# Performance work log

Measured on AMD Instinct MI355X. Metric: run time of the kernel, lower is better.

## Reference

```python
import jax, jax.numpy as jnp
import numpy as np
from functools import partial

N = 10  # n_qubits (static)


def _rx(state, w, theta, n):
    # state: [B, 2^n] complex64; RX(theta) on wire w (wire 0 = most significant)
    B = state.shape[0]
    st = state.reshape(B, 2 ** w, 2, 2 ** (n - 1 - w))
    half = jnp.asarray(theta, state.real.dtype) * 0.5
    c = jnp.cos(half).reshape(-1, 1, 1)
    s = jnp.sin(half).reshape(-1, 1, 1)
    s0, s1 = st[:, :, 0], st[:, :, 1]
    n0 = c * s0 - 1j * s * s1
    n1 = -1j * s * s0 + c * s1
    return jnp.stack([n0, n1], axis=2).reshape(B, 2 ** n)


def _cnot(state, control, target, n):
    B = state.shape[0]
    a, bb = (control, target) if control < target else (target, control)
    st = state.reshape(B, 2 ** a, 2, 2 ** (bb - a - 1), 2, 2 ** (n - 1 - bb))
    if control == a:
        # control is axis 2, target axis 4: flip target where control==1
        c1 = jnp.flip(st[:, :, 1], axis=3)
        st = jnp.stack([st[:, :, 0], c1], axis=2)
    else:
        # control is axis 4, target axis 2: flip axis-2 slice where control==1
        c1 = jnp.flip(st[:, :, :, :, 1], axis=1)
        st = jnp.stack([st[:, :, :, :, 0], c1], axis=4)
    return st.reshape(B, 2 ** n)


def _expect_z(state, n):
    B = state.shape[0]
    probs = jnp.abs(state) ** 2  # [B, 2^n]
    es = []
    for w in range(n):
        p = probs.reshape(B, 2 ** w, 2, 2 ** (n - 1 - w))
        es.append(p[:, :, 0].sum((1, 2)) - p[:, :, 1].sum((1, 2)))
    return jnp.stack(es, axis=1)  # [B, n]


def _qlayer(x, theta, n):
    # x: [B, n] encoder angles; theta: [n] trainable RX angles
    B = x.shape[0]
    state = jnp.zeros((B, 2 ** n), jnp.complex64).at[:, 0].set(1.0)
    for w in range(n):
        state = _rx(state, w, x[:, w], n)
    for w in range(n):
        state = _rx(state, w, theta[w], n)
    for w in range(n - 1):
        state = _cnot(state, w, w + 1, n)
    state = _cnot(state, n - 1, 0, n)
    return _expect_z(state, n)


def setup_inputs() -> dict:
    key = jax.random.key(0)
    k1, k2, k3, k4 = jax.random.split(key, 4)
    T, B, D, H = 64, 256, 246, N
    inputs = jax.random.normal(k1, (T, B, D), jnp.float32)
    fan_in = D + H
    W = jax.random.normal(k2, (4, N, fan_in), jnp.float32) / np.sqrt(fan_in)
    b = jax.random.normal(k3, (4, N), jnp.float32) * 0.01
    thetas = jax.random.normal(k4, (4, N), jnp.float32)
    return {"inputs": inputs, "W": W, "b": b, "thetas": thetas}


def reference(inputs, W, b, thetas):
    T, B, D = inputs.shape
    H = thetas.shape[-1]
    qlayer4 = jax.vmap(partial(_qlayer, n=N))  # over the 4 gates

    def step(carry, x_t):
        hx, cx = carry
        comb = jnp.concatenate([x_t, hx], axis=1)          # [B, D+H]
        z = jnp.einsum('bi,goi->gbo', comb, W) + b[:, None, :]  # [4, B, n]
        gates = qlayer4(z, thetas)                          # [4, B, n]
        f = jax.nn.sigmoid(gates[0])
        i = jax.nn.sigmoid(gates[1])
        g = jnp.tanh(gates[2])
        o = jax.nn.sigmoid(gates[3])
        cx = f * cx + i * g
        hx = o * jnp.tanh(cx)
        return (hx, cx), hx

    hx0 = jnp.zeros((B, H), inputs.dtype)
    cx0 = jnp.zeros((B, H), inputs.dtype)
    (hx, cx), outputs = jax.lax.scan(step, (hx0, cx0), inputs)
    return outputs, hx, cx
```

## Files before the change

### kernel.cpp

```cpp
#include <hip/hip_runtime.h>
#include <hip/hip_bf16.h>

#define D_IN   246
#define NW     10
#define NG     4
#define FANIN  256
#define BATCH  256
#define TSTEPS 64
#define ZSTR   42
#define WP_ELEMS (NG * D_IN * 16)

__global__ __launch_bounds__(256) void k_wt(const float* __restrict__ W,
                                            float* __restrict__ Wp) {
    int e = blockIdx.x * 256 + threadIdx.x;
    if (e >= WP_ELEMS) return;
    int o = e & 15;
    int i = (e >> 4) % D_IN;
    int g = e / (16 * D_IN);
    float v = (o < NW) ? W[(g * NW + o) * FANIN + i] : 0.f;
    Wp[e] = v;
}

template <int CTRL>
__device__ __forceinline__ float dpp_shr_mul(float p) {
    int up = __builtin_amdgcn_update_dpp(__float_as_int(1.0f), __float_as_int(p),
                                         CTRL, 0xF, 0xF, false);
    return p * __int_as_float(up);
}

__global__ __launch_bounds__(256) void k_fused(
    const float* __restrict__ x,
    const float* __restrict__ Wp,
    const float* __restrict__ bias,
    const float* __restrict__ theta,
    const float* __restrict__ W,
    float* __restrict__ out,
    float* __restrict__ hxout,
    float* __restrict__ cxout)
{
    const int b    = blockIdx.x;
    const int tid  = threadIdx.x;
    const int lane = tid & 63;
    const int wv   = __builtin_amdgcn_readfirstlane(tid >> 6);

    __shared__ float xl[64 * D_IN];
    __shared__ float zl[TSTEPS * ZSTR];

    for (int row = wv; row < 64; row += 4) {
        const float* src = x + ((size_t)row * BATCH + b) * D_IN;
        float* dst = xl + row * D_IN;
        for (int j = lane; j < 123; j += 64) {
            float2 v = *reinterpret_cast<const float2*>(src + 2 * j);
            *reinterpret_cast<float2*>(dst + 2 * j) = v;
        }
    }
    __syncthreads();

    {
        const int g = wv;
        float acc[NW];
#pragma unroll
        for (int o = 0; o < NW; ++o)
            acc[o] = bias[g * NW + o] + theta[g * NW + o];

        const float* wg = Wp + g * D_IN * 16;
        const float* xr = xl + lane * D_IN;

#pragma unroll 4
        for (int ii = 0; ii < 123; ++ii) {
            float2 xv = *reinterpret_cast<const float2*>(xr + 2 * ii);
#pragma unroll
            for (int o = 0; o < NW; ++o) {
                acc[o] = fmaf(xv.x, wg[(2 * ii) * 16 + o], acc[o]);
                acc[o] = fmaf(xv.y, wg[(2 * ii + 1) * 16 + o], acc[o]);
            }
        }

        float* zo = zl + lane * ZSTR + g * NW;
#pragma unroll
        for (int q = 0; q < 5; ++q)
            *reinterpret_cast<float2*>(zo + 2 * q) = make_float2(acc[2 * q], acc[2 * q + 1]);
    }
    __syncthreads();

    if (wv != 0) return;

    const int r   = lane >> 4;
    const int o   = lane & 15;
    const bool act = (o < NW);
    const int oc  = act ? o : 0;
    const int cidx = r * NW + oc;

    float wh[NW];
#pragma unroll
    for (int j = 0; j < NW; ++j)
        wh[j] = W[(r * NW + oc) * FANIN + D_IN + j];

    const float am = (r == 2) ? 2.f : 1.f;
    const float vm = (r == 2) ? 2.f : 1.f;
    const float vc = (r == 2) ? -1.f : 0.f;
    const int idx1 = (lane ^ 16) << 2;
    const int idx2 = (lane ^ 32) << 2;
    const int idx3 = (lane ^ 48) << 2;
    const bool q1 = (r & 1) != 0;
    const bool q2 = (r & 2) != 0;

    float hx_s[NW];
#pragma unroll
    for (int j = 0; j < NW; ++j) hx_s[j] = 0.f;

    float cx = 0.f, hv = 0.f;
    float zc = zl[cidx];

    for (int t = 0; t < TSTEPS; ++t) {
        float zn = zl[((t + 1) & 63) * ZSTR + cidx];

        float s0 = zc, s1 = 0.f;
#pragma unroll
        for (int j = 0; j < 5; ++j) {
            s0 = fmaf(hx_s[2 * j],     wh[2 * j],     s0);
            s1 = fmaf(hx_s[2 * j + 1], wh[2 * j + 1], s1);
        }
        float z = s0 + s1;

        float cv = __cosf(z);

        float p = cv;
        p = dpp_shr_mul<0x111>(p);
        p = dpp_shr_mul<0x112>(p);
        p = dpp_shr_mul<0x114>(p);
        p = dpp_shr_mul<0x118>(p);

        float e  = __expf(-(p * am));
        float sg = __fdividef(1.f, 1.f + e);
        float val = fmaf(sg, vm, vc);

        int vi = __float_as_int(val);
        float a1 = __int_as_float(__builtin_amdgcn_ds_bpermute(idx1, vi));
        float a2 = __int_as_float(__builtin_amdgcn_ds_bpermute(idx2, vi));
        float a3 = __int_as_float(__builtin_amdgcn_ds_bpermute(idx3, vi));

        float fv = q2 ? (q1 ? a3 : a2) : (q1 ? a1 : val);
        float iv = q2 ? (q1 ? a2 : a3) : (q1 ? val : a1);
        float gv = q2 ? (q1 ? a1 : val) : (q1 ? a3 : a2);
        float ov = q2 ? (q1 ? val : a1) : (q1 ? a2 : a3);

        cx = fmaf(fv, cx, iv * gv);
        float e2 = __expf(cx + cx);
        float th = 1.f - __fdividef(2.f, 1.f + e2);
        hv = ov * th;

        if (r == 0 && act) out[((size_t)t * BATCH + b) * NW + o] = hv;

#pragma unroll
        for (int j = 0; j < NW; ++j)
            hx_s[j] = __int_as_float(__builtin_amdgcn_readlane(__float_as_int(hv), j));

        zc = zn;
    }

    if (r == 0 && act) {
        hxout[b * NW + o] = hv;
        cxout[b * NW + o] = cx;
    }
}

extern "C" void kernel_launch(void* const* d_in, const int* in_sizes, int n_in,
                              void* d_out, int out_size, void* d_ws, size_t ws_size,
                              hipStream_t stream) {
    const float* x     = (const float*)d_in[0];
    const float* W     = (const float*)d_in[1];
    const float* bias  = (const float*)d_in[2];
    const float* theta = (const float*)d_in[3];

    float* out   = (float*)d_out;
    float* hxout = out + (size_t)TSTEPS * BATCH * NW;
    float* cxout = hxout + (size_t)BATCH * NW;

    float* Wp = (float*)d_ws;

    k_wt<<<(WP_ELEMS + 255) / 256, 256, 0, stream>>>(W, Wp);
    k_fused<<<BATCH, 256, 0, stream>>>(x, Wp, bias, theta, W, out, hxout, cxout);
}
```

Before: 121.8 us.

## Split input projection across 8 waves and compute all four gates per lane

The kernel now launches 512 threads per block, splitting the 246-wide input projection into two K-halves across 8 waves and reducing the partial sums through shared memory. The recurrent phase is restructured so each lane evaluates all four gates for its hidden unit. This replaces the cross-row ds_bpermute exchange with four independent cos/DPP product chains, and the four z values are read as one float4 from a gate-interleaved LDS layout. The goal is to shorten the precompute phase and the serial per-step latency. The cost is an extra barrier, more LDS use, and more per-lane work in the recurrence.

```diff
diff --git a/kernel.cpp b/kernel.cpp
--- a/kernel.cpp
+++ b/kernel.cpp
@@ -4,10 +4,10 @@
 #define D_IN   246
 #define NW     10
 #define NG     4
+#define NOUT   40
 #define FANIN  256
 #define BATCH  256
 #define TSTEPS 64
-#define ZSTR   42
 #define WP_ELEMS (NG * D_IN * 16)
 
 __global__ __launch_bounds__(256) void k_wt(const float* __restrict__ W,
@@ -28,7 +28,7 @@
     return p * __int_as_float(up);
 }
 
-__global__ __launch_bounds__(256) void k_fused(
+__global__ __launch_bounds__(512) void k_fused(
     const float* __restrict__ x,
     const float* __restrict__ Wp,
     const float* __restrict__ bias,
@@ -42,11 +42,25 @@
     const int tid  = threadIdx.x;
     const int lane = tid & 63;
     const int wv   = __builtin_amdgcn_readfirstlane(tid >> 6);
+    const int g    = wv & 3;
+    const int kh   = wv >> 2;
 
     __shared__ float xl[64 * D_IN];
-    __shared__ float zl[TSTEPS * ZSTR];
+    __shared__ float pr[NG][64][NW];
+    __shared__ float zl[TSTEPS * NOUT];
 
-    for (int row = wv; row < 64; row += 4) {
+    const int o16 = lane & 15;
+    const int oc  = (o16 < NW) ? o16 : 0;
+    float wh[NG][NW];
+    if (wv == 0) {
+#pragma unroll
+        for (int gg = 0; gg < NG; ++gg)
+#pragma unroll
+            for (int j = 0; j < NW; ++j)
+                wh[gg][j] = W[(gg * NW + oc) * FANIN + D_IN + j];
+    }
+
+    for (int row = wv; row < 64; row += 8) {
         const float* src = x + ((size_t)row * BATCH + b) * D_IN;
         float* dst = xl + row * D_IN;
         for (int j = lane; j < 123; j += 64) {
@@ -57,111 +71,96 @@
     __syncthreads();
 
     {
-        const int g = wv;
+        const int khbase = kh ? 124 : 0;
+        const int npairs = kh ? 61 : 62;
+
         float acc[NW];
 #pragma unroll
-        for (int o = 0; o < NW; ++o)
-            acc[o] = bias[g * NW + o] + theta[g * NW + o];
+        for (int o = 0; o < NW; ++o) acc[o] = 0.f;
 
-        const float* wg = Wp + g * D_IN * 16;
-        const float* xr = xl + lane * D_IN;
+        const float* wg = Wp + (g * D_IN + khbase) * 16;
+        const float* xr = xl + lane * D_IN + khbase;
 
 #pragma unroll 4
-        for (int ii = 0; ii < 123; ++ii) {
+        for (int ii = 0; ii < npairs; ++ii) {
             float2 xv = *reinterpret_cast<const float2*>(xr + 2 * ii);
 #pragma unroll
             for (int o = 0; o < NW; ++o) {
-                acc[o] = fmaf(xv.x, wg[(2 * ii) * 16 + o], acc[o]);
+                acc[o] = fmaf(xv.x, wg[(2 * ii)     * 16 + o], acc[o]);
                 acc[o] = fmaf(xv.y, wg[(2 * ii + 1) * 16 + o], acc[o]);
             }
         }
 
-        float* zo = zl + lane * ZSTR + g * NW;
+        if (kh == 1) {
 #pragma unroll
-        for (int q = 0; q < 5; ++q)
-            *reinterpret_cast<float2*>(zo + 2 * q) = make_float2(acc[2 * q], acc[2 * q + 1]);
+            for (int o = 0; o < NW; ++o) pr[g][lane][o] = acc[o];
+        }
+        __syncthreads();
+
+        if (kh == 0) {
+#pragma unroll
+            for (int o = 0; o < NW; ++o) {
+                float v = acc[o] + pr[g][lane][o] + bias[g * NW + o] + theta[g * NW + o];
+                zl[lane * NOUT + o * NG + g] = v;
+            }
+        }
     }
     __syncthreads();
-
     if (wv != 0) return;
-
-    const int r   = lane >> 4;
-    const int o   = lane & 15;
-    const bool act = (o < NW);
-    const int oc  = act ? o : 0;
-    const int cidx = r * NW + oc;
-
-    float wh[NW];
-#pragma unroll
-    for (int j = 0; j < NW; ++j)
-        wh[j] = W[(r * NW + oc) * FANIN + D_IN + j];
-
-    const float am = (r == 2) ? 2.f : 1.f;
-    const float vm = (r == 2) ? 2.f : 1.f;
-    const float vc = (r == 2) ? -1.f : 0.f;
-    const int idx1 = (lane ^ 16) << 2;
-    const int idx2 = (lane ^ 32) << 2;
-    const int idx3 = (lane ^ 48) << 2;
-    const bool q1 = (r & 1) != 0;
-    const bool q2 = (r & 2) != 0;
 
     float hx_s[NW];
 #pragma unroll
     for (int j = 0; j < NW; ++j) hx_s[j] = 0.f;
+    float cx = 0.f, hv = 0.f;
 
-    float cx = 0.f, hv = 0.f;
-    float zc = zl[cidx];
+    const float* zrow = zl + oc * NG;
+    float4 zn = *reinterpret_cast<const float4*>(zrow);
+    float* outp = out + (size_t)b * NW + oc;
 
     for (int t = 0; t < TSTEPS; ++t) {
-        float zn = zl[((t + 1) & 63) * ZSTR + cidx];
+        float4 zc4 = zn;
+        zn = *reinterpret_cast<const float4*>(zrow + ((t + 1) & 63) * NOUT);
 
-        float s0 = zc, s1 = 0.f;
+        float z0 = zc4.x, z1 = zc4.y, z2 = zc4.z, z3 = zc4.w;
 #pragma unroll
-        for (int j = 0; j < 5; ++j) {
-            s0 = fmaf(hx_s[2 * j],     wh[2 * j],     s0);
-            s1 = fmaf(hx_s[2 * j + 1], wh[2 * j + 1], s1);
+        for (int j = 0; j < NW; ++j) {
+            z0 = fmaf(hx_s[j], wh[0][j], z0);
+            z1 = fmaf(hx_s[j], wh[1][j], z1);
+            z2 = fmaf(hx_s[j], wh[2][j], z2);
+            z3 = fmaf(hx_s[j], wh[3][j], z3);
         }
-        float z = s0 + s1;
 
-        float cv = __cosf(z);
+        float p0 = __cosf(z0), p1 = __cosf(z1), p2 = __cosf(z2), p3 = __cosf(z3);
 
-        float p = cv;
-        p = dpp_shr_mul<0x111>(p);
-        p = dpp_shr_mul<0x112>(p);
-        p = dpp_shr_mul<0x114>(p);
-        p = dpp_shr_mul<0x118>(p);
+        p0 = dpp_shr_mul<0x111>(p0); p1 = dpp_shr_mul<0x111>(p1);
+        p2 = dpp_shr_mul<0x111>(p2); p3 = dpp_shr_mul<0x111>(p3);
+        p0 = dpp_shr_mul<0x112>(p0); p1 = dpp_shr_mul<0x112>(p1);
+        p2 = dpp_shr_mul<0x112>(p2); p3 = dpp_shr_mul<0x112>(p3);
+        p0 = dpp_shr_mul<0x114>(p0); p1 = dpp_shr_mul<0x114>(p1);
+        p2 = dpp_shr_mul<0x114>(p2); p3 = dpp_shr_mul<0x114>(p3);
+        p0 = dpp_shr_mul<0x118>(p0); p1 = dpp_shr_mul<0x118>(p1);
+        p2 = dpp_shr_mul<0x118>(p2); p3 = dpp_shr_mul<0x118>(p3);
 
-        float e  = __expf(-(p * am));
-        float sg = __fdividef(1.f, 1.f + e);
-        float val = fmaf(sg, vm, vc);
+        float fg  = __fdividef(1.f, 1.f + __expf(-p0));
+        float ig  = __fdividef(1.f, 1.f + __expf(-p1));
+        float gg2 = 2.f * __fdividef(1.f, 1.f + __expf(-2.f * p2)) - 1.f;
+        float og  = __fdividef(1.f, 1.f + __expf(-p3));
 
-        int vi = __float_as_int(val);
-        float a1 = __int_as_float(__builtin_amdgcn_ds_bpermute(idx1, vi));
-        float a2 = __int_as_float(__builtin_amdgcn_ds_bpermute(idx2, vi));
-        float a3 = __int_as_float(__builtin_amdgcn_ds_bpermute(idx3, vi));
-
-        float fv = q2 ? (q1 ? a3 : a2) : (q1 ? a1 : val);
-        float iv = q2 ? (q1 ? a2 : a3) : (q1 ? val : a1);
-        float gv = q2 ? (q1 ? a1 : val) : (q1 ? a3 : a2);
-        float ov = q2 ? (q1 ? val : a1) : (q1 ? a2 : a3);
-
-        cx = fmaf(fv, cx, iv * gv);
+        cx = fmaf(fg, cx, ig * gg2);
         float e2 = __expf(cx + cx);
         float th = 1.f - __fdividef(2.f, 1.f + e2);
-        hv = ov * th;
+        hv = og * th;
 
-        if (r == 0 && act) out[((size_t)t * BATCH + b) * NW + o] = hv;
+        if (lane < NW) outp[(size_t)t * (BATCH * NW)] = hv;
 
 #pragma unroll
         for (int j = 0; j < NW; ++j)
             hx_s[j] = __int_as_float(__builtin_amdgcn_readlane(__float_as_int(hv), j));
-
-        zc = zn;
     }
 
-    if (r == 0 && act) {
-        hxout[b * NW + o] = hv;
-        cxout[b * NW + o] = cx;
+    if (lane < NW) {
+        hxout[b * NW + lane] = hv;
+        cxout[b * NW + lane] = cx;
     }
 }
 
@@ -180,5 +179,5 @@
     float* Wp = (float*)d_ws;
 
     k_wt<<<(WP_ELEMS + 255) / 256, 256, 0, stream>>>(W, Wp);
-    k_fused<<<BATCH, 256, 0, stream>>>(x, Wp, bias, theta, W, out, hxout, cxout);
+    k_fused<<<BATCH, 512, 0, stream>>>(x, Wp, bias, theta, W, out, hxout, cxout);
 }
```

Result: faster. 116.6 us (-4.2%).
